# Kernel tuning notes

Measured on AMD Instinct MI355X. Metric: run time of the kernel, lower is better.

The kernel has to match this reference:

```python
import jax, jax.numpy as jnp
import numpy as np

B, T, N_EMBD, HEAD = 4, 4096, 1024, 64


def setup_inputs() -> dict:
    key = jax.random.key(0)
    k1, k2, k3, k4 = jax.random.split(key, 4)
    x = jax.random.normal(k1, (B, T, N_EMBD), dtype=jnp.float32)
    # nn.Linear weights, stored as [in, out] so y = x @ W
    s = 1.0 / np.sqrt(N_EMBD)
    Wq = jax.random.uniform(k2, (N_EMBD, HEAD), dtype=jnp.float32, minval=-s, maxval=s)
    Wk = jax.random.uniform(k3, (N_EMBD, HEAD), dtype=jnp.float32, minval=-s, maxval=s)
    Wv = jax.random.uniform(k4, (N_EMBD, HEAD), dtype=jnp.float32, minval=-s, maxval=s)
    return {"x": x, "Wq": Wq, "Wk": Wk, "Wv": Wv}


def reference(x, Wq, Wk, Wv):
    # x: [B, T, C] with C = n_embd; note: original scales by sqrt(C), not sqrt(head_size)
    T_, C = x.shape[1], x.shape[2]
    q = x @ Wq            # [B, T, H]
    k = x @ Wk            # [B, T, H]
    v = x @ Wv            # [B, T, H]
    scale = 1.0 / jnp.sqrt(jnp.asarray(C, dtype=x.dtype))
    w = jnp.einsum('bqh,bkh->bqk', q, k) * scale  # [B, T, T]
    causal = jnp.tril(jnp.ones((T_, T_), dtype=bool))
    w = jnp.where(causal, w, -jnp.inf)
    attn = jax.nn.softmax(w, axis=-1)
    # dropout in eval mode (identity) for deterministic reference
    return attn @ v       # [B, T, H]
```

## Files before the change

kernel.cpp:

```cpp
#include <hip/hip_runtime.h>

constexpr int B_  = 4;
constexpr int T_  = 4096;
constexpr int C_  = 1024;
constexpr int H_  = 64;
constexpr int BT_ = B_ * T_;
constexpr int NUNIT_ = 1152;

typedef __attribute__((ext_vector_type(4))) float f32x4;
typedef __attribute__((ext_vector_type(8))) short bf16x8;
typedef __attribute__((ext_vector_type(8))) unsigned short u16x8;
typedef __attribute__((ext_vector_type(4))) unsigned short u16x4;

__device__ __forceinline__ unsigned short f32_to_bf16(float f) {
    union { float f; unsigned int u; } v;
    v.f = f;
    unsigned int r = v.u + 0x7FFFu + ((v.u >> 16) & 1u);
    return (unsigned short)(r >> 16);
}
__device__ __forceinline__ float bf16_to_f32(unsigned short us) {
    union { unsigned int u; float f; } v;
    v.u = (unsigned int)us << 16;
    return v.f;
}
__device__ __forceinline__ float exp2_hw(float x) {
    return __builtin_amdgcn_exp2f(x);
}

__global__ __launch_bounds__(256) void wconv_kernel(
    const float* __restrict__ Wq, const float* __restrict__ Wk,
    const float* __restrict__ Wv, unsigned short* __restrict__ Wt)
{
    const int tid  = threadIdx.x;
    const int wid  = blockIdx.x * 4 + (tid >> 6);
    const int lane = tid & 63;
    const int q    = lane >> 4, c = lane & 15;
    const int ntile = wid >> 5;
    const int kstep = wid & 31;
    const int n = ntile * 16 + c;
    const int m = n >> 6;
    const float* W = (m == 0) ? Wq : (m == 1) ? Wk : Wv;
    const int ncol = n & 63;
    const int k0 = kstep * 32 + q * 8;
    u16x8 pk;
#pragma unroll
    for (int j = 0; j < 8; j++) pk[j] = f32_to_bf16(W[(size_t)(k0 + j) * H_ + ncol]);
    *(u16x8*)(Wt + (size_t)wid * 512 + lane * 8) = pk;
}

__global__ __launch_bounds__(128, 4) void proj_kernel(
    const float* __restrict__ x, const unsigned short* __restrict__ Wt,
    unsigned short* __restrict__ Qf, unsigned short* __restrict__ Kf,
    unsigned short* __restrict__ Vf)
{
    __shared__ __align__(16) unsigned short xs[2][16][72];
    const int t     = threadIdx.x;
    const int mtile = blockIdx.x & 1023;
    const int half_ = blockIdx.x >> 10;
    const int r0    = mtile * 16;
    const int w     = t >> 6;
    const int lane  = t & 63;
    const int quad  = lane >> 4;
    const int c     = lane & 15;
    const int nh    = half_ * 96 + w * 48;
    const int row   = t >> 3;
    const int koff  = (t & 7) * 4;

    f32x4 acc[3];
#pragma unroll
    for (int j = 0; j < 3; j++) acc[j] = {0.f, 0.f, 0.f, 0.f};

    const float* xp = x + (size_t)(r0 + row) * C_ + koff;
    f32x4 v0 = *(const f32x4*)xp;
    f32x4 v1 = *(const f32x4*)(xp + 32);

    int p = 0;
    for (int kk = 0; kk < C_; kk += 64) {
        u16x4 pk0, pk1;
#pragma unroll
        for (int i = 0; i < 4; i++) {
            pk0[i] = f32_to_bf16(v0[i]);
            pk1[i] = f32_to_bf16(v1[i]);
        }
        *(u16x4*)&xs[p][row][koff]      = pk0;
        *(u16x4*)&xs[p][row][koff + 32] = pk1;
        __syncthreads();
        if (kk + 64 < C_) {
            v0 = *(const f32x4*)(xp + kk + 64);
            v1 = *(const f32x4*)(xp + kk + 96);
        }
#pragma unroll
        for (int ks = 0; ks < 64; ks += 32) {
            const bf16x8 a0 = *(const bf16x8*)&xs[p][c][ks + quad * 8];
            const unsigned short* bp =
                Wt + ((size_t)(nh >> 4) * 32 + ((kk + ks) >> 5)) * 512 + lane * 8;
#pragma unroll
            for (int j = 0; j < 3; j++) {
                const bf16x8 bj = *(const bf16x8*)(bp + (size_t)j * 32 * 512);
                acc[j] = __builtin_amdgcn_mfma_f32_16x16x32_bf16(a0, bj, acc[j], 0, 0, 0);
            }
        }
        p ^= 1;
    }

    const int S   = r0;
    const int bS  = S >> 12;
    const int cc0 = quad * 4;
#pragma unroll
    for (int j = 0; j < 3; j++) {
        const int nt = nh + j * 16;
        if (nt < 128) {
            const int d0 = (nt < 64) ? nt : nt - 64;
            unsigned short* base = (nt < 64) ? Qf : Kf;
            const int t16  = (S & 4095) >> 4;
            const int half = d0 >> 5;
            const int q8   = ((d0 >> 4) & 1) * 2 + (c >> 3);
            const int j8   = c & 7;
            unsigned short* pq = base + ((size_t)(bS * 256 + t16)) * 1024
                               + half * 512 + q8 * 128 + j8;
#pragma unroll
            for (int r = 0; r < 4; r++) pq[(cc0 + r) * 8] = f32_to_bf16(acc[j][r]);
        } else {
            const int d0  = nt - 128;
            const int k32 = (S & 4095) >> 5;
            const int ht  = d0 >> 4;
            const int sq  = (S & 31) >> 3;
            unsigned short* pv = Vf + (((size_t)(bS * 128 + k32)) * 4 + ht) * 512 + c * 8;
#pragma unroll
            for (int r = 0; r < 4; r++) {
                const int cc = cc0 + r;
                pv[(sq + (cc >> 3)) * 128 + (cc & 7)] = f32_to_bf16(acc[j][r]);
            }
        }
    }
}

__global__ __launch_bounds__(256) void attn_kernel(
    const unsigned short* __restrict__ Qf, const unsigned short* __restrict__ Kf,
    const unsigned short* __restrict__ Vf, unsigned short* __restrict__ Opg,
    float* __restrict__ mlg)
{
    __shared__ __align__(16) unsigned short Pb[4][16][72];
    const int tid  = threadIdx.x;
    const int w    = tid >> 6;
    const int lane = tid & 63;
    const int quad = lane >> 4;
    const int c    = lane & 15;
    const int bid  = blockIdx.x;
    const int qt   = 255 - (bid & 255);
    const int ks   = bid >> 8;
    const int g    = qt >> 5;
    if (ks > g) return;
    const int b    = w;
    const int q0   = qt * 16;
    const int k0   = ks * 512;
    const int kend = (q0 + 15 < k0 + 511) ? q0 + 15 : k0 + 511;

    const unsigned short* qp = Qf + ((size_t)b * 256 + qt) * 1024 + lane * 8;
    const bf16x8 qB0 = *(const bf16x8*)qp;
    const bf16x8 qB1 = *(const bf16x8*)(qp + 512);

    f32x4 O[4];
#pragma unroll
    for (int tt = 0; tt < 4; tt++) O[tt] = {0.f, 0.f, 0.f, 0.f};
    float m = -1e30f, ls = 0.f;
    const float scale2 = 0.045084436f;

    unsigned short* P = &Pb[w][0][0];
    const int prow = c * 72;

    for (int kb = k0; kb <= kend; kb += 64) {
        const unsigned short* kfb = Kf + ((size_t)b * 256 + (kb >> 4)) * 1024 + lane * 8;
        f32x4 S[4];
#pragma unroll
        for (int tt = 0; tt < 4; tt++) {
            const bf16x8 kA0 = *(const bf16x8*)(kfb + tt * 1024);
            const bf16x8 kA1 = *(const bf16x8*)(kfb + tt * 1024 + 512);
            f32x4 s = {0.f, 0.f, 0.f, 0.f};
            s = __builtin_amdgcn_mfma_f32_16x16x32_bf16(kA0, qB0, s, 0, 0, 0);
            s = __builtin_amdgcn_mfma_f32_16x16x32_bf16(kA1, qB1, s, 0, 0, 0);
            S[tt] = s;
        }
        float sc[16];
        if (kb + 63 > q0) {
#pragma unroll
            for (int tt = 0; tt < 4; tt++)
#pragma unroll
                for (int r = 0; r < 4; r++) {
                    const int key = kb + tt * 16 + quad * 4 + r;
                    sc[tt * 4 + r] = (key > q0 + c) ? -1e30f : S[tt][r] * scale2;
                }
        } else {
#pragma unroll
            for (int tt = 0; tt < 4; tt++)
#pragma unroll
                for (int r = 0; r < 4; r++) sc[tt * 4 + r] = S[tt][r] * scale2;
        }
        float mx = sc[0];
#pragma unroll
        for (int i = 1; i < 16; i++) mx = fmaxf(mx, sc[i]);
        mx = fmaxf(mx, __shfl_xor(mx, 16));
        mx = fmaxf(mx, __shfl_xor(mx, 32));
        const float mn    = fmaxf(m, mx);
        const float alpha = exp2_hw(m - mn);
        m = mn;
        float lsum = 0.f;
#pragma unroll
        for (int tt = 0; tt < 4; tt++) {
            u16x4 pk;
#pragma unroll
            for (int r = 0; r < 4; r++) {
                const float e = exp2_hw(sc[tt * 4 + r] - mn);
                lsum += e;
                pk[r] = f32_to_bf16(e);
            }
            *(u16x4*)(P + prow + tt * 16 + quad * 4) = pk;
        }
        ls = ls * alpha + lsum;
#pragma unroll
        for (int tt = 0; tt < 4; tt++)
#pragma unroll
            for (int r = 0; r < 4; r++) O[tt][r] *= alpha;

        const bf16x8 pB0 = *(const bf16x8*)(P + prow + quad * 8);
        const bf16x8 pB1 = *(const bf16x8*)(P + prow + 32 + quad * 8);

        const unsigned short* vfb = Vf + ((size_t)b * 128 + (kb >> 5)) * 2048 + lane * 8;
#pragma unroll
        for (int tt = 0; tt < 4; tt++) {
            const bf16x8 vA0 = *(const bf16x8*)(vfb + tt * 512);
            const bf16x8 vA1 = *(const bf16x8*)(vfb + 2048 + tt * 512);
            O[tt] = __builtin_amdgcn_mfma_f32_16x16x32_bf16(vA0, pB0, O[tt], 0, 0, 0);
            O[tt] = __builtin_amdgcn_mfma_f32_16x16x32_bf16(vA1, pB1, O[tt], 0, 0, 0);
        }
    }

    ls += __shfl_xor(ls, 16);
    ls += __shfl_xor(ls, 32);

    const size_t ustore = (size_t)b * NUNIT_ + qt + 16 * g * (g - 1) + g * (qt & 31) + ks;
#pragma unroll
    for (int tt = 0; tt < 4; tt++) {
        u16x4 pk;
#pragma unroll
        for (int r = 0; r < 4; r++) pk[r] = f32_to_bf16(O[tt][r]);
        *(u16x4*)(Opg + ustore * 1024 + c * 64 + tt * 16 + quad * 4) = pk;
    }
    if (lane < 16) {
        mlg[ustore * 32 + c]      = m;
        mlg[ustore * 32 + 16 + c] = ls;
    }
}

__global__ __launch_bounds__(256) void merge_kernel(
    const unsigned short* __restrict__ Opg, const float* __restrict__ mlg,
    float* __restrict__ out)
{
    const int idx = blockIdx.x;
    const int b   = idx >> 8;
    const int qt  = idx & 255;
    const int g   = qt >> 5;
    const int nseg = g + 1;
    const size_t base = (size_t)b * NUNIT_ + qt + 16 * g * (g - 1) + g * (qt & 31);
    const int t  = threadIdx.x;
    const int h  = t & 63;
    const int rg = t >> 6;
#pragma unroll
    for (int i = 0; i < 4; i++) {
        const int row = rg * 4 + i;
        float M = -1e30f;
        for (int s = 0; s < nseg; s++) M = fmaxf(M, mlg[(base + s) * 32 + row]);
        float L = 0.f, val = 0.f;
        for (int s = 0; s < nseg; s++) {
            const float e = exp2_hw(mlg[(base + s) * 32 + row] - M);
            L   = fmaf(mlg[(base + s) * 32 + 16 + row], e, L);
            val = fmaf(bf16_to_f32(Opg[(base + s) * 1024 + row * 64 + h]), e, val);
        }
        out[((size_t)b * T_ + qt * 16 + row) * H_ + h] = val / L;
    }
}

extern "C" void kernel_launch(void* const* d_in, const int* in_sizes, int n_in,
                              void* d_out, int out_size, void* d_ws, size_t ws_size,
                              hipStream_t stream) {
    const float* x  = (const float*)d_in[0];
    const float* Wq = (const float*)d_in[1];
    const float* Wk = (const float*)d_in[2];
    const float* Wv = (const float*)d_in[3];
    float* out = (float*)d_out;

    unsigned short* Qf = (unsigned short*)d_ws;
    unsigned short* Kf = Qf + (size_t)BT_ * H_;
    unsigned short* Vf = Kf + (size_t)BT_ * H_;
    unsigned short* Wt = Vf + (size_t)BT_ * H_;
    unsigned short* Opg = Wt + (size_t)192 * C_;
    float*          mlg = (float*)(Opg + (size_t)B_ * NUNIT_ * 1024);

    wconv_kernel<<<96, 256, 0, stream>>>(Wq, Wk, Wv, Wt);
    proj_kernel<<<2048, 128, 0, stream>>>(x, Wt, Qf, Kf, Vf);
    attn_kernel<<<2048, 256, 0, stream>>>(Qf, Kf, Vf, Opg, mlg);
    merge_kernel<<<1024, 256, 0, stream>>>(Opg, mlg, out);
}
```

Before: 170.4 us.

## Merge projection halves per block and prefetch K tiles in attention loop

The projection kernel now runs 256-thread blocks that compute all 192 output columns for a 16-row tile, so each x row is loaded and converted to bf16 once instead of twice. The attention kernel keeps the next K tile in registers, loading it while the current tile is processed, to hide global load latency behind softmax and PV work. The online-softmax rescale of O and the running sum is skipped when no lane's max increases, and the max and sum reductions are written as trees. These add register pressure and a wave-wide vote branch in exchange for fewer redundant loads and fewer multiplies.

```diff
diff --git a/kernel.cpp b/kernel.cpp
--- a/kernel.cpp
+++ b/kernel.cpp
@@ -48,23 +48,21 @@
     *(u16x8*)(Wt + (size_t)wid * 512 + lane * 8) = pk;
 }
 
-__global__ __launch_bounds__(128, 4) void proj_kernel(
+__global__ __launch_bounds__(256, 4) void proj_kernel(
     const float* __restrict__ x, const unsigned short* __restrict__ Wt,
     unsigned short* __restrict__ Qf, unsigned short* __restrict__ Kf,
     unsigned short* __restrict__ Vf)
 {
     __shared__ __align__(16) unsigned short xs[2][16][72];
-    const int t     = threadIdx.x;
-    const int mtile = blockIdx.x & 1023;
-    const int half_ = blockIdx.x >> 10;
-    const int r0    = mtile * 16;
-    const int w     = t >> 6;
-    const int lane  = t & 63;
-    const int quad  = lane >> 4;
-    const int c     = lane & 15;
-    const int nh    = half_ * 96 + w * 48;
-    const int row   = t >> 3;
-    const int koff  = (t & 7) * 4;
+    const int t    = threadIdx.x;
+    const int r0   = blockIdx.x * 16;
+    const int w    = t >> 6;
+    const int lane = t & 63;
+    const int quad = lane >> 4;
+    const int c    = lane & 15;
+    const int nh   = w * 48;
+    const int row  = t >> 4;
+    const int koff = (t & 15) * 4;
 
     f32x4 acc[3];
 #pragma unroll
@@ -72,23 +70,15 @@
 
     const float* xp = x + (size_t)(r0 + row) * C_ + koff;
     f32x4 v0 = *(const f32x4*)xp;
-    f32x4 v1 = *(const f32x4*)(xp + 32);
 
     int p = 0;
     for (int kk = 0; kk < C_; kk += 64) {
-        u16x4 pk0, pk1;
-#pragma unroll
-        for (int i = 0; i < 4; i++) {
-            pk0[i] = f32_to_bf16(v0[i]);
-            pk1[i] = f32_to_bf16(v1[i]);
-        }
-        *(u16x4*)&xs[p][row][koff]      = pk0;
-        *(u16x4*)&xs[p][row][koff + 32] = pk1;
+        u16x4 pk0;
+#pragma unroll
+        for (int i = 0; i < 4; i++) pk0[i] = f32_to_bf16(v0[i]);
+        *(u16x4*)&xs[p][row][koff] = pk0;
         __syncthreads();
-        if (kk + 64 < C_) {
-            v0 = *(const f32x4*)(xp + kk + 64);
-            v1 = *(const f32x4*)(xp + kk + 96);
-        }
+        if (kk + 64 < C_) v0 = *(const f32x4*)(xp + kk + 64);
 #pragma unroll
         for (int ks = 0; ks < 64; ks += 32) {
             const bf16x8 a0 = *(const bf16x8*)&xs[p][c][ks + quad * 8];
@@ -169,58 +159,86 @@
     unsigned short* P = &Pb[w][0][0];
     const int prow = c * 72;
 
+    bf16x8 kC[8];
+    {
+        const unsigned short* kfb = Kf + ((size_t)b * 256 + (k0 >> 4)) * 1024 + lane * 8;
+#pragma unroll
+        for (int i = 0; i < 4; i++) {
+            kC[2 * i]     = *(const bf16x8*)(kfb + i * 1024);
+            kC[2 * i + 1] = *(const bf16x8*)(kfb + i * 1024 + 512);
+        }
+    }
+
     for (int kb = k0; kb <= kend; kb += 64) {
-        const unsigned short* kfb = Kf + ((size_t)b * 256 + (kb >> 4)) * 1024 + lane * 8;
         f32x4 S[4];
 #pragma unroll
         for (int tt = 0; tt < 4; tt++) {
-            const bf16x8 kA0 = *(const bf16x8*)(kfb + tt * 1024);
-            const bf16x8 kA1 = *(const bf16x8*)(kfb + tt * 1024 + 512);
             f32x4 s = {0.f, 0.f, 0.f, 0.f};
-            s = __builtin_amdgcn_mfma_f32_16x16x32_bf16(kA0, qB0, s, 0, 0, 0);
-            s = __builtin_amdgcn_mfma_f32_16x16x32_bf16(kA1, qB1, s, 0, 0, 0);
+            s = __builtin_amdgcn_mfma_f32_16x16x32_bf16(kC[2 * tt],     qB0, s, 0, 0, 0);
+            s = __builtin_amdgcn_mfma_f32_16x16x32_bf16(kC[2 * tt + 1], qB1, s, 0, 0, 0);
             S[tt] = s;
         }
-        float sc[16];
+        if (kb + 64 <= kend) {
+            const unsigned short* kfb =
+                Kf + ((size_t)b * 256 + ((kb + 64) >> 4)) * 1024 + lane * 8;
+#pragma unroll
+            for (int i = 0; i < 4; i++) {
+                kC[2 * i]     = *(const bf16x8*)(kfb + i * 1024);
+                kC[2 * i + 1] = *(const bf16x8*)(kfb + i * 1024 + 512);
+            }
+        }
+
         if (kb + 63 > q0) {
 #pragma unroll
             for (int tt = 0; tt < 4; tt++)
 #pragma unroll
                 for (int r = 0; r < 4; r++) {
                     const int key = kb + tt * 16 + quad * 4 + r;
-                    sc[tt * 4 + r] = (key > q0 + c) ? -1e30f : S[tt][r] * scale2;
+                    const float v = S[tt][r] * scale2;
+                    S[tt][r] = (key > q0 + c) ? -1e30f : v;
                 }
         } else {
 #pragma unroll
             for (int tt = 0; tt < 4; tt++)
 #pragma unroll
-                for (int r = 0; r < 4; r++) sc[tt * 4 + r] = S[tt][r] * scale2;
-        }
-        float mx = sc[0];
-#pragma unroll
-        for (int i = 1; i < 16; i++) mx = fmaxf(mx, sc[i]);
+                for (int r = 0; r < 4; r++) S[tt][r] *= scale2;
+        }
+
+        float t0 = fmaxf(fmaxf(S[0][0], S[0][1]), fmaxf(S[0][2], S[0][3]));
+        float t1 = fmaxf(fmaxf(S[1][0], S[1][1]), fmaxf(S[1][2], S[1][3]));
+        float t2 = fmaxf(fmaxf(S[2][0], S[2][1]), fmaxf(S[2][2], S[2][3]));
+        float t3 = fmaxf(fmaxf(S[3][0], S[3][1]), fmaxf(S[3][2], S[3][3]));
+        float mx = fmaxf(fmaxf(t0, t1), fmaxf(t2, t3));
         mx = fmaxf(mx, __shfl_xor(mx, 16));
         mx = fmaxf(mx, __shfl_xor(mx, 32));
-        const float mn    = fmaxf(m, mx);
-        const float alpha = exp2_hw(m - mn);
-        m = mn;
-        float lsum = 0.f;
+
+        if (__any(mx > m)) {
+            const float mn    = fmaxf(m, mx);
+            const float alpha = exp2_hw(m - mn);
+            m = mn;
+            ls *= alpha;
+#pragma unroll
+            for (int tt = 0; tt < 4; tt++)
+#pragma unroll
+                for (int r = 0; r < 4; r++) O[tt][r] *= alpha;
+        }
+
+        float lp0 = 0.f, lp1 = 0.f, lp2 = 0.f, lp3 = 0.f;
 #pragma unroll
         for (int tt = 0; tt < 4; tt++) {
             u16x4 pk;
+            float l = 0.f;
 #pragma unroll
             for (int r = 0; r < 4; r++) {
-                const float e = exp2_hw(sc[tt * 4 + r] - mn);
-                lsum += e;
+                const float e = exp2_hw(S[tt][r] - m);
+                l += e;
                 pk[r] = f32_to_bf16(e);
             }
+            if (tt == 0) lp0 = l; else if (tt == 1) lp1 = l;
+            else if (tt == 2) lp2 = l; else lp3 = l;
             *(u16x4*)(P + prow + tt * 16 + quad * 4) = pk;
         }
-        ls = ls * alpha + lsum;
-#pragma unroll
-        for (int tt = 0; tt < 4; tt++)
-#pragma unroll
-            for (int r = 0; r < 4; r++) O[tt][r] *= alpha;
+        ls += (lp0 + lp1) + (lp2 + lp3);
 
         const bf16x8 pB0 = *(const bf16x8*)(P + prow + quad * 8);
         const bf16x8 pB1 = *(const bf16x8*)(P + prow + 32 + quad * 8);
@@ -297,7 +315,7 @@
     float*          mlg = (float*)(Opg + (size_t)B_ * NUNIT_ * 1024);
 
     wconv_kernel<<<96, 256, 0, stream>>>(Wq, Wk, Wv, Wt);
-    proj_kernel<<<2048, 128, 0, stream>>>(x, Wt, Qf, Kf, Vf);
+    proj_kernel<<<1024, 256, 0, stream>>>(x, Wt, Qf, Kf, Vf);
     attn_kernel<<<2048, 256, 0, stream>>>(Qf, Kf, Vf, Opg, mlg);
     merge_kernel<<<1024, 256, 0, stream>>>(Opg, mlg, out);
 }
```

After: 173.8 us. Within noise of the previous version (+2.0%).
